# Optimization experiments

Measured on AMD Instinct MI355X. Metric: run time of the kernel, lower is better.

Reference implementation:

```python
import jax, jax.numpy as jnp
import numpy as np

N = 8192
NUM_FEAT = 512
NUM_HIDDENS = 128


def _mlp_params(key, fin, fh):
    k1, k2, k3, k4 = jax.random.split(key, 4)
    s1 = 1.0 / np.sqrt(fin)
    s2 = 1.0 / np.sqrt(fh)
    W1 = jax.random.uniform(k1, (fin, fh), jnp.float32, -s1, s1)
    b1 = jax.random.uniform(k2, (fh,), jnp.float32, -s1, s1)
    W2 = jax.random.uniform(k3, (fh, fh), jnp.float32, -s2, s2)
    b2 = jax.random.uniform(k4, (fh,), jnp.float32, -s2, s2)
    return W1, b1, W2, b2


def setup_inputs() -> dict:
    key = jax.random.key(0)
    ks = jax.random.split(key, 9)
    feat = jax.random.normal(ks[0], (N, NUM_FEAT), jnp.float32)
    adj = jax.random.uniform(ks[1], (N, N), jnp.float32)
    aa = jax.random.uniform(ks[2], (N, N), jnp.float32)
    mod = jax.random.normal(ks[3], (N, N), jnp.float32)
    Wl1, bl1, Wl2, bl2 = _mlp_params(ks[4], NUM_FEAT, NUM_HIDDENS)
    Wu1, bu1, Wu2, bu2 = _mlp_params(ks[5], NUM_FEAT, NUM_HIDDENS)
    Wa1, ba1, Wa2, ba2 = _mlp_params(ks[6], NUM_FEAT, NUM_HIDDENS)
    Wm1, bm1, Wm2, bm2 = _mlp_params(ks[7], NUM_FEAT, NUM_HIDDENS)
    ws = jnp.zeros((3,), jnp.float32)  # nn.init.zeros_(weighted_sum)
    return dict(feat=feat, adj=adj, aa=aa, mod=mod,
                Wl1=Wl1, bl1=bl1, Wl2=Wl2, bl2=bl2,
                Wu1=Wu1, bu1=bu1, Wu2=Wu2, bu2=bu2,
                Wa1=Wa1, ba1=ba1, Wa2=Wa2, ba2=ba2,
                Wm1=Wm1, bm1=bm1, Wm2=Wm2, bm2=bm2,
                ws=ws)


def _latent(feat, W1, b1, W2, b2):
    h = jax.nn.relu(feat @ W1 + b1)
    return h @ W2 + b2  # [N, H]


def reference(feat, adj, aa, mod,
              Wl1, bl1, Wl2, bl2,
              Wu1, bu1, Wu2, bu2,
              Wa1, ba1, Wa2, ba2,
              Wm1, bm1, Wm2, bm2, ws):
    lat_link = _latent(feat, Wl1, bl1, Wl2, bl2)
    lat_aa = _latent(feat, Wa1, ba1, Wa2, ba2)
    lat_mod = _latent(feat, Wm1, bm1, Wm2, bm2)
    lat_unlink = _latent(feat, Wu1, bu1, Wu2, bu2)

    link_ctx = jax.nn.sigmoid(lat_link @ lat_link.T)          # [N, N]
    aa_ctx = jax.nn.sigmoid((lat_aa @ lat_aa.T) * aa)         # [N, N]
    mod_ctx = jax.nn.sigmoid((lat_mod @ lat_mod.T) * mod)     # [N, N]

    w = jax.nn.softmax(ws)  # [3]
    # cat(..., dim=2) @ w  ==  weighted sum of the three contexts
    weight_link = w[0] * link_ctx + w[1] * aa_ctx + w[2] * mod_ctx

    weight_unlink = jax.nn.sigmoid(lat_unlink @ lat_unlink.T)
    return (weight_link - weight_unlink) * adj + weight_unlink
```

## Files before the change

### kernel.cpp

```cpp
#include <hip/hip_runtime.h>


typedef __attribute__((ext_vector_type(8))) short short8;
typedef __attribute__((ext_vector_type(4))) float f32x4;

__device__ __forceinline__ unsigned short f2bf(float x) {
  union { float f; unsigned u; } v; v.f = x;
  unsigned u = v.u + 0x7FFFu + ((v.u >> 16) & 1u);
  return (unsigned short)(u >> 16);
}

__device__ __forceinline__ float sigf(float x) {
  float e = __builtin_amdgcn_exp2f(-1.4426950408889634f * x);
  return __builtin_amdgcn_rcpf(1.0f + e);
}

__device__ __forceinline__ void gload_lds16u(const unsigned short* g, unsigned short* l) {
  __builtin_amdgcn_global_load_lds(
      (const __attribute__((address_space(1))) void*)g,
      (__attribute__((address_space(3))) void*)l, 16, 0, 0);
}

__device__ __forceinline__ unsigned lds_off(const void* p) {
  return (unsigned)(uintptr_t)(const __attribute__((address_space(3))) void*)p;
}
__device__ __forceinline__ short8 ds_read_frag(unsigned a) {
  short8 d;
  asm volatile("ds_read_b128 %0, %1" : "=v"(d) : "v"(a));
  return d;
}

__global__ __launch_bounds__(256) void k_featfrag(const float* __restrict__ feat,
                                                  unsigned short* __restrict__ dst) {
  int t = blockIdx.x * 256 + threadIdx.x;
  int row = t >> 6, kc = t & 63;
  const float4* s = reinterpret_cast<const float4*>(feat + row * 512 + kc * 8);
  float4 v0 = s[0], v1 = s[1];
  short8 o;
  o[0] = f2bf(v0.x); o[1] = f2bf(v0.y); o[2] = f2bf(v0.z); o[3] = f2bf(v0.w);
  o[4] = f2bf(v1.x); o[5] = f2bf(v1.y); o[6] = f2bf(v1.z); o[7] = f2bf(v1.w);
  int mb = row >> 4, kk = kc >> 2;
  int lane = ((kc & 3) << 4) | (row & 15);
  *reinterpret_cast<short8*>(dst + ((size_t)((mb * 16 + kk) * 64 + lane)) * 8) = o;
}

__global__ __launch_bounds__(256) void k_wfrag(
    const float* __restrict__ w1_0, const float* __restrict__ w1_1,
    const float* __restrict__ w1_2, const float* __restrict__ w1_3,
    const float* __restrict__ w2_0, const float* __restrict__ w2_1,
    const float* __restrict__ w2_2, const float* __restrict__ w2_3,
    unsigned short* __restrict__ w1f, unsigned short* __restrict__ w2f) {
  int t = blockIdx.x * 256 + threadIdx.x;
  if (t < 32768) {
    int lane = t & 63, nb = (t >> 6) & 7, kk = (t >> 9) & 15, g = t >> 13;
    const float* W = g == 0 ? w1_0 : g == 1 ? w1_1 : g == 2 ? w1_2 : w1_3;
    int q = lane >> 4, r = lane & 15;
    int col = nb * 16 + r;
    short8 o;
#pragma unroll
    for (int j = 0; j < 8; ++j) o[j] = f2bf(W[(kk * 32 + q * 8 + j) * 128 + col]);
    *reinterpret_cast<short8*>(w1f + (size_t)t * 8) = o;
  } else if (t < 40960) {
    int t2 = t - 32768;
    int lane = t2 & 63, nb = (t2 >> 6) & 7, kk = (t2 >> 9) & 3, g = t2 >> 11;
    const float* W = g == 0 ? w2_0 : g == 1 ? w2_1 : g == 2 ? w2_2 : w2_3;
    int q = lane >> 4, r = lane & 15;
    int col = nb * 16 + r;
    short8 o;
#pragma unroll
    for (int j = 0; j < 8; ++j) o[j] = f2bf(W[(kk * 32 + q * 8 + j) * 128 + col]);
    *reinterpret_cast<short8*>(w2f + (size_t)t2 * 8) = o;
  }
}

__global__ __launch_bounds__(256) void k_gemm1(
    const unsigned short* __restrict__ featf, const unsigned short* __restrict__ w1f,
    const float* __restrict__ b1_0, const float* __restrict__ b1_1,
    const float* __restrict__ b1_2, const float* __restrict__ b1_3,
    unsigned short* __restrict__ hfrag) {
  int bi = blockIdx.x, g = blockIdx.y;
  int lane = threadIdx.x & 63, w = threadIdx.x >> 6;
  int wm = w >> 1, wn = w & 1;
  int q = lane >> 4, r = lane & 15;
  int mbase = 8 * bi + 4 * wm;

  f32x4 s[4][4];
#pragma unroll
  for (int mi = 0; mi < 4; ++mi)
#pragma unroll
    for (int nj = 0; nj < 4; ++nj) s[mi][nj] = (f32x4){0.f, 0.f, 0.f, 0.f};

  for (int kk = 0; kk < 16; ++kk) {
    short8 a[4], b[4];
#pragma unroll
    for (int mi = 0; mi < 4; ++mi)
      a[mi] = *reinterpret_cast<const short8*>(
          featf + ((size_t)(((mbase + mi) * 16 + kk) * 64 + lane)) * 8);
#pragma unroll
    for (int nj = 0; nj < 4; ++nj)
      b[nj] = *reinterpret_cast<const short8*>(
          w1f + ((size_t)(((g * 16 + kk) * 8 + 4 * wn + nj) * 64 + lane)) * 8);
#pragma unroll
    for (int mi = 0; mi < 4; ++mi)
#pragma unroll
      for (int nj = 0; nj < 4; ++nj)
        s[mi][nj] = __builtin_amdgcn_mfma_f32_16x16x32_bf16(a[mi], b[nj], s[mi][nj], 0, 0, 0);
  }

  const float* b1 = g == 0 ? b1_0 : g == 1 ? b1_1 : g == 2 ? b1_2 : b1_3;
#pragma unroll
  for (int nj = 0; nj < 4; ++nj) {
    int cl = 64 * wn + 16 * nj + r;
    float bias = b1[cl];
    int Cg = 128 * g + cl;
    int kkd = Cg >> 5;
    int lane2hi = ((Cg >> 3) & 3) << 4;
    int j2 = Cg & 7;
#pragma unroll
    for (int mi = 0; mi < 4; ++mi) {
#pragma unroll
      for (int v = 0; v < 4; ++v) {
        int R = 128 * bi + 64 * wm + 16 * mi + 4 * q + v;
        float val = fmaxf(s[mi][nj][v] + bias, 0.0f);
        int mb = R >> 4;
        int lane2 = lane2hi | (R & 15);
        hfrag[((size_t)((mb * 16 + kkd) * 64 + lane2)) * 8 + j2] = f2bf(val);
      }
    }
  }
}

__global__ __launch_bounds__(256) void k_gemm2(
    const unsigned short* __restrict__ hfrag, const unsigned short* __restrict__ w2f,
    const float* __restrict__ b2_0, const float* __restrict__ b2_1,
    const float* __restrict__ b2_2, const float* __restrict__ b2_3,
    unsigned short* __restrict__ latf) {
  int bi = blockIdx.x, g = blockIdx.y;
  int lane = threadIdx.x & 63, w = threadIdx.x >> 6;
  int wm = w >> 1, wn = w & 1;
  int q = lane >> 4, r = lane & 15;
  int mbase = 8 * bi + 4 * wm;

  f32x4 s[4][4];
#pragma unroll
  for (int mi = 0; mi < 4; ++mi)
#pragma unroll
    for (int nj = 0; nj < 4; ++nj) s[mi][nj] = (f32x4){0.f, 0.f, 0.f, 0.f};

#pragma unroll
  for (int kk = 0; kk < 4; ++kk) {
    short8 a[4], b[4];
#pragma unroll
    for (int mi = 0; mi < 4; ++mi)
      a[mi] = *reinterpret_cast<const short8*>(
          hfrag + ((size_t)(((mbase + mi) * 16 + 4 * g + kk) * 64 + lane)) * 8);
#pragma unroll
    for (int nj = 0; nj < 4; ++nj)
      b[nj] = *reinterpret_cast<const short8*>(
          w2f + ((size_t)(((g * 4 + kk) * 8 + 4 * wn + nj) * 64 + lane)) * 8);
#pragma unroll
    for (int mi = 0; mi < 4; ++mi)
#pragma unroll
      for (int nj = 0; nj < 4; ++nj)
        s[mi][nj] = __builtin_amdgcn_mfma_f32_16x16x32_bf16(a[mi], b[nj], s[mi][nj], 0, 0, 0);
  }

  const float* b2 = g == 0 ? b2_0 : g == 1 ? b2_1 : g == 2 ? b2_2 : b2_3;
#pragma unroll
  for (int nj = 0; nj < 4; ++nj) {
    int cl = 64 * wn + 16 * nj + r;
    float bias = b2[cl];
    int kkd = cl >> 5;
    int lane2hi = ((cl >> 3) & 3) << 4;
    int j2 = cl & 7;
#pragma unroll
    for (int mi = 0; mi < 4; ++mi) {
#pragma unroll
      for (int v = 0; v < 4; ++v) {
        int R = 128 * bi + 64 * wm + 16 * mi + 4 * q + v;
        float val = s[mi][nj][v] + bias;
        int mb = R >> 4;
        int lane2 = lane2hi | (R & 15);
        latf[((size_t)(((g * 512 + mb) * 4 + kkd) * 64 + lane2)) * 8 + j2] = f2bf(val);
      }
    }
  }
}


#define VLD4(dst, p, OFF) \
  asm volatile("global_load_dwordx4 %0, %1, off offset:" OFF : "=v"(dst) : "v"(p))

#define LOADG(F, BASE, G)                                                     \
  do {                                                                        \
    const unsigned short* _p = (BASE) + (size_t)(G) * GS;                     \
    VLD4(F[0], _p, "0");    VLD4(F[1], _p, "1024");                           \
    VLD4(F[2], _p, "2048"); VLD4(F[3], _p, "3072");                           \
  } while (0)

#define GRAMG(SG, F, G)                                                       \
  do {                                                                        \
    short8 _i0 = ds_read_frag(fib + ((G) * 4 + 0) * 1024u + l16);             \
    short8 _i1 = ds_read_frag(fib + ((G) * 4 + 1) * 1024u + l16);             \
    short8 _i2 = ds_read_frag(fib + ((G) * 4 + 2) * 1024u + l16);             \
    short8 _i3 = ds_read_frag(fib + ((G) * 4 + 3) * 1024u + l16);             \
    asm volatile("s_waitcnt lgkmcnt(0)" ::: "memory");                        \
    __builtin_amdgcn_sched_barrier(0);                                        \
    SG = (f32x4){0.f, 0.f, 0.f, 0.f};                                         \
    SG = __builtin_amdgcn_mfma_f32_16x16x32_bf16(F[0], _i0, SG, 0, 0, 0);     \
    SG = __builtin_amdgcn_mfma_f32_16x16x32_bf16(F[1], _i1, SG, 0, 0, 0);     \
    SG = __builtin_amdgcn_mfma_f32_16x16x32_bf16(F[2], _i2, SG, 0, 0, 0);     \
    SG = __builtin_amdgcn_mfma_f32_16x16x32_bf16(F[3], _i3, SG, 0, 0, 0);     \
  } while (0)

#define STEP(S, EWCa, EWCm, EWCj, EWNa, EWNm, EWNj)                           \
  do {                                                                        \
    const unsigned short* fjbase =                                            \
        latf + (size_t)(cb0 + (S) * 4 + w) * 2048 + (size_t)lane * 8;         \
    f32x4 sg, o4;                                                             \
                                                     \
    LOADG(fjB, fjbase, 1);                                                    \
    asm volatile("s_waitcnt vmcnt(8)" ::: "memory");                          \
    __builtin_amdgcn_sched_barrier(0);                                        \
    GRAMG(sg, fjA, 0);                                                        \
    o4[0] = w0 * sigf(sg[0]); o4[1] = w0 * sigf(sg[1]);                       \
    o4[2] = w0 * sigf(sg[2]); o4[3] = w0 * sigf(sg[3]);                       \
                                                     \
    LOADG(fjA, fjbase, 2);                                                    \
    asm volatile("s_waitcnt vmcnt(4)" ::: "memory");                          \
    __builtin_amdgcn_sched_barrier(0);                                        \
    GRAMG(sg, fjB, 1);                                                        \
    o4[0] += w1 * sigf(sg[0] * EWCa[0]); o4[1] += w1 * sigf(sg[1] * EWCa[1]); \
    o4[2] += w1 * sigf(sg[2] * EWCa[2]); o4[3] += w1 * sigf(sg[3] * EWCa[3]); \
                                                     \
    LOADG(fjB, fjbase, 3);                                                    \
    asm volatile("s_waitcnt vmcnt(4)" ::: "memory");                          \
    __builtin_amdgcn_sched_barrier(0);                                        \
    GRAMG(sg, fjA, 2);                                                        \
    o4[0] += w2 * sigf(sg[0] * EWCm[0]); o4[1] += w2 * sigf(sg[1] * EWCm[1]); \
    o4[2] += w2 * sigf(sg[2] * EWCm[2]); o4[3] += w2 * sigf(sg[3] * EWCm[3]); \
                  \
    {                                                                         \
      const unsigned short* _nb = fjbase + 4 * 2048;    \
      LOADG(fjA, _nb, 0);                                                     \
      int _sn = ((S) + 1 < 32) ? (S) + 1 : (S);                               \
      const float* _ea = aa + ewoff + (size_t)_sn * 64;                       \
      const float* _em = mod + ewoff + (size_t)_sn * 64;                      \
      const float* _ej = adj + ewoff + (size_t)_sn * 64;                      \
      VLD4(EWNa, _ea, "0"); VLD4(EWNm, _em, "0"); VLD4(EWNj, _ej, "0");       \
    }                                                                         \
    asm volatile("s_waitcnt vmcnt(7)" ::: "memory");                          \
    __builtin_amdgcn_sched_barrier(0);                                        \
    GRAMG(sg, fjB, 3);                                                        \
    f32x4 res;                                                                \
    {                                                                         \
      float u0 = sigf(sg[0]), u1 = sigf(sg[1]);                               \
      float u2 = sigf(sg[2]), u3 = sigf(sg[3]);                               \
      res[0] = EWCj[0] * (o4[0] - u0) + u0;                                   \
      res[1] = EWCj[1] * (o4[1] - u1) + u1;                                   \
      res[2] = EWCj[2] * (o4[2] - u2) + u2;                                   \
      res[3] = EWCj[3] * (o4[3] - u3) + u3;                                   \
    }                                                                         \
    {                                                                         \
      float* _op = out + ewoff + (size_t)(S) * 64;                            \
      asm volatile("global_store_dwordx4 %0, %1, off" ::"v"(_op), "v"(res)    \
                   : "memory");                                               \
    }                                                                         \
  } while (0)

__global__ __launch_bounds__(256, 4) void k_ctx(
    const unsigned short* __restrict__ latf,
    const float* __restrict__ adj, const float* __restrict__ aa,
    const float* __restrict__ mod, const float* __restrict__ wsv,
    float* __restrict__ out) {
  __shared__ unsigned short fi_lds[8192];

  const int bid = blockIdx.x;
  const int cs = bid & 3;
  const int mb = bid >> 2;
  const int lane = threadIdx.x & 63, w = threadIdx.x >> 6;
  const int q = lane >> 4, r = lane & 15;

  float s0w = wsv[0], s1w = wsv[1], s2w = wsv[2];
  float mx = fmaxf(fmaxf(s0w, s1w), s2w);
  float e0 = __builtin_amdgcn_exp2f(1.4426950408889634f * (s0w - mx));
  float e1 = __builtin_amdgcn_exp2f(1.4426950408889634f * (s1w - mx));
  float e2 = __builtin_amdgcn_exp2f(1.4426950408889634f * (s2w - mx));
  float inv = __builtin_amdgcn_rcpf(e0 + e1 + e2);
  float w0 = e0 * inv, w1 = e1 * inv, w2 = e2 * inv;

  const size_t GS = (size_t)512 * 2048;
  const int cb0 = cs * 128;

  const size_t ewoff = (size_t)(mb * 16 + r) * 8192 + (size_t)cs * 2048
                     + (size_t)(16 * w + 4 * q);

#pragma unroll
  for (int kk = 0; kk < 4; ++kk)
    gload_lds16u(latf + GS * w + (size_t)(mb * 4 + kk) * 512 + lane * 8,
                 &fi_lds[(w * 4 + kk) * 512]);

  short8 fjA[4], fjB[4];
  f32x4 ewAa, ewAm, ewAj, ewBa, ewBm, ewBj;
  {
    const unsigned short* fjbase0 =
        latf + (size_t)(cb0 + w) * 2048 + (size_t)lane * 8;
    LOADG(fjA, fjbase0, 0);
  }
  VLD4(ewAa, (aa + ewoff), "0");
  VLD4(ewAm, (mod + ewoff), "0");
  VLD4(ewAj, (adj + ewoff), "0");
  asm volatile("s_waitcnt vmcnt(0)" ::: "memory");
  __builtin_amdgcn_s_barrier();

  const unsigned fib = lds_off(fi_lds);
  const unsigned l16 = (unsigned)lane * 16u;

#pragma unroll 1
  for (int s = 0; s < 32; s += 2) {
    STEP(s, ewAa, ewAm, ewAj, ewBa, ewBm, ewBj);
    STEP(s + 1, ewBa, ewBm, ewBj, ewAa, ewAm, ewAj);
  }
}

extern "C" void kernel_launch(void* const* d_in, const int* in_sizes, int n_in,
                              void* d_out, int out_size, void* d_ws, size_t ws_size,
                              hipStream_t stream) {
  const float* feat = (const float*)d_in[0];
  const float* adj  = (const float*)d_in[1];
  const float* aa   = (const float*)d_in[2];
  const float* mod  = (const float*)d_in[3];
  const float* W1g[4] = {(const float*)d_in[4], (const float*)d_in[12],
                         (const float*)d_in[16], (const float*)d_in[8]};
  const float* b1g[4] = {(const float*)d_in[5], (const float*)d_in[13],
                         (const float*)d_in[17], (const float*)d_in[9]};
  const float* W2g[4] = {(const float*)d_in[6], (const float*)d_in[14],
                         (const float*)d_in[18], (const float*)d_in[10]};
  const float* b2g[4] = {(const float*)d_in[7], (const float*)d_in[15],
                         (const float*)d_in[19], (const float*)d_in[11]};
  const float* wsv = (const float*)d_in[20];
  float* out = (float*)d_out;

  unsigned short* featf = (unsigned short*)d_ws;
  unsigned short* hfrag = featf + 4194304;
  unsigned short* latf  = hfrag + 4194304;
  unsigned short* w1f   = latf + 4194304;
  unsigned short* w2f   = w1f + 262144;
  if (ws_size < 25821184) return;

  k_featfrag<<<2048, 256, 0, stream>>>(feat, featf);
  k_wfrag<<<160, 256, 0, stream>>>(W1g[0], W1g[1], W1g[2], W1g[3],
                                   W2g[0], W2g[1], W2g[2], W2g[3], w1f, w2f);
  k_gemm1<<<dim3(64, 4), 256, 0, stream>>>(featf, w1f, b1g[0], b1g[1], b1g[2], b1g[3], hfrag);
  k_gemm2<<<dim3(64, 4), 256, 0, stream>>>(hfrag, w2f, b2g[0], b2g[1], b2g[2], b2g[3], latf);
  k_ctx<<<2048, 256, 0, stream>>>(latf, adj, aa, mod, wsv, out);
}
```

Measured before the change: 441.0 us.

## Keep row fragments in registers and stream shared column fragments through triple-buffered LDS

```diff
diff --git a/kernel.cpp b/kernel.cpp
--- a/kernel.cpp
+++ b/kernel.cpp
@@ -188,70 +188,57 @@
 }
 
 
+#define FILD(dst, p, OFF) \
+  asm volatile("global_load_dwordx4 %0, %1, off offset:" OFF : "=v"(dst) : "v"(p))
 #define VLD4(dst, p, OFF) \
   asm volatile("global_load_dwordx4 %0, %1, off offset:" OFF : "=v"(dst) : "v"(p))
 
-#define LOADG(F, BASE, G)                                                     \
+#define GRAMF(SG, G, FJC)                                                     \
   do {                                                                        \
-    const unsigned short* _p = (BASE) + (size_t)(G) * GS;                     \
-    VLD4(F[0], _p, "0");    VLD4(F[1], _p, "1024");                           \
-    VLD4(F[2], _p, "2048"); VLD4(F[3], _p, "3072");                           \
-  } while (0)
-
-#define GRAMG(SG, F, G)                                                       \
-  do {                                                                        \
-    short8 _i0 = ds_read_frag(fib + ((G) * 4 + 0) * 1024u + l16);             \
-    short8 _i1 = ds_read_frag(fib + ((G) * 4 + 1) * 1024u + l16);             \
-    short8 _i2 = ds_read_frag(fib + ((G) * 4 + 2) * 1024u + l16);             \
-    short8 _i3 = ds_read_frag(fib + ((G) * 4 + 3) * 1024u + l16);             \
+    short8 _j0 = ds_read_frag((FJC) + ((G) * 4 + 0) * 1024u + l16);           \
+    short8 _j1 = ds_read_frag((FJC) + ((G) * 4 + 1) * 1024u + l16);           \
+    short8 _j2 = ds_read_frag((FJC) + ((G) * 4 + 2) * 1024u + l16);           \
+    short8 _j3 = ds_read_frag((FJC) + ((G) * 4 + 3) * 1024u + l16);           \
     asm volatile("s_waitcnt lgkmcnt(0)" ::: "memory");                        \
     __builtin_amdgcn_sched_barrier(0);                                        \
     SG = (f32x4){0.f, 0.f, 0.f, 0.f};                                         \
-    SG = __builtin_amdgcn_mfma_f32_16x16x32_bf16(F[0], _i0, SG, 0, 0, 0);     \
-    SG = __builtin_amdgcn_mfma_f32_16x16x32_bf16(F[1], _i1, SG, 0, 0, 0);     \
-    SG = __builtin_amdgcn_mfma_f32_16x16x32_bf16(F[2], _i2, SG, 0, 0, 0);     \
-    SG = __builtin_amdgcn_mfma_f32_16x16x32_bf16(F[3], _i3, SG, 0, 0, 0);     \
+    SG = __builtin_amdgcn_mfma_f32_16x16x32_bf16(_j0, fi[G][0], SG, 0, 0, 0); \
+    SG = __builtin_amdgcn_mfma_f32_16x16x32_bf16(_j1, fi[G][1], SG, 0, 0, 0); \
+    SG = __builtin_amdgcn_mfma_f32_16x16x32_bf16(_j2, fi[G][2], SG, 0, 0, 0); \
+    SG = __builtin_amdgcn_mfma_f32_16x16x32_bf16(_j3, fi[G][3], SG, 0, 0, 0); \
   } while (0)
 
 #define STEP(S, EWCa, EWCm, EWCj, EWNa, EWNm, EWNj)                           \
   do {                                                                        \
-    const unsigned short* fjbase =                                            \
-        latf + (size_t)(cb0 + (S) * 4 + w) * 2048 + (size_t)lane * 8;         \
+    int _bf = (br == 2) ? 0 : br + 1;                                         \
+    int _sn = ((S) < 63) ? (S) + 1 : 63;                                      \
+    {                                                                         \
+      const unsigned short* _fp = latf + GS * w                               \
+          + ((size_t)((tj0 + _sn) * 4) << 9) + (size_t)lane * 8;              \
+      gload_lds16u(_fp,        &fj_lds[_bf][w * 4 + 0][0]);                   \
+      gload_lds16u(_fp + 512,  &fj_lds[_bf][w * 4 + 1][0]);                   \
+      gload_lds16u(_fp + 1024, &fj_lds[_bf][w * 4 + 2][0]);                   \
+      gload_lds16u(_fp + 1536, &fj_lds[_bf][w * 4 + 3][0]);                   \
+      VLD4(EWNa, (aa + ewoff + (size_t)_sn * 16), "0");                       \
+      VLD4(EWNm, (mod + ewoff + (size_t)_sn * 16), "0");                      \
+      VLD4(EWNj, (adj + ewoff + (size_t)_sn * 16), "0");                      \
+    }                                                                         \
+    __builtin_amdgcn_sched_barrier(0);                                        \
+          \
+    asm volatile("s_waitcnt vmcnt(7)" ::: "memory");                          \
+    __builtin_amdgcn_s_barrier();                                             \
+    const unsigned _fjc = fjb + (unsigned)br * 16384u;                        \
     f32x4 sg, o4;                                                             \
-                                                     \
-    LOADG(fjB, fjbase, 1);                                                    \
-    asm volatile("s_waitcnt vmcnt(8)" ::: "memory");                          \
-    __builtin_amdgcn_sched_barrier(0);                                        \
-    GRAMG(sg, fjA, 0);                                                        \
+    GRAMF(sg, 0, _fjc);                                                       \
     o4[0] = w0 * sigf(sg[0]); o4[1] = w0 * sigf(sg[1]);                       \
     o4[2] = w0 * sigf(sg[2]); o4[3] = w0 * sigf(sg[3]);                       \
-                                                     \
-    LOADG(fjA, fjbase, 2);                                                    \
-    asm volatile("s_waitcnt vmcnt(4)" ::: "memory");                          \
-    __builtin_amdgcn_sched_barrier(0);                                        \
-    GRAMG(sg, fjB, 1);                                                        \
+    GRAMF(sg, 1, _fjc);                                                       \
     o4[0] += w1 * sigf(sg[0] * EWCa[0]); o4[1] += w1 * sigf(sg[1] * EWCa[1]); \
     o4[2] += w1 * sigf(sg[2] * EWCa[2]); o4[3] += w1 * sigf(sg[3] * EWCa[3]); \
-                                                     \
-    LOADG(fjB, fjbase, 3);                                                    \
-    asm volatile("s_waitcnt vmcnt(4)" ::: "memory");                          \
-    __builtin_amdgcn_sched_barrier(0);                                        \
-    GRAMG(sg, fjA, 2);                                                        \
+    GRAMF(sg, 2, _fjc);                                                       \
     o4[0] += w2 * sigf(sg[0] * EWCm[0]); o4[1] += w2 * sigf(sg[1] * EWCm[1]); \
     o4[2] += w2 * sigf(sg[2] * EWCm[2]); o4[3] += w2 * sigf(sg[3] * EWCm[3]); \
-                  \
-    {                                                                         \
-      const unsigned short* _nb = fjbase + 4 * 2048;    \
-      LOADG(fjA, _nb, 0);                                                     \
-      int _sn = ((S) + 1 < 32) ? (S) + 1 : (S);                               \
-      const float* _ea = aa + ewoff + (size_t)_sn * 64;                       \
-      const float* _em = mod + ewoff + (size_t)_sn * 64;                      \
-      const float* _ej = adj + ewoff + (size_t)_sn * 64;                      \
-      VLD4(EWNa, _ea, "0"); VLD4(EWNm, _em, "0"); VLD4(EWNj, _ej, "0");       \
-    }                                                                         \
-    asm volatile("s_waitcnt vmcnt(7)" ::: "memory");                          \
-    __builtin_amdgcn_sched_barrier(0);                                        \
-    GRAMG(sg, fjB, 3);                                                        \
+    GRAMF(sg, 3, _fjc);                                                       \
     f32x4 res;                                                                \
     {                                                                         \
       float u0 = sigf(sg[0]), u1 = sigf(sg[1]);                               \
@@ -262,24 +249,26 @@
       res[3] = EWCj[3] * (o4[3] - u3) + u3;                                   \
     }                                                                         \
     {                                                                         \
-      float* _op = out + ewoff + (size_t)(S) * 64;                            \
+      float* _op = out + ewoff + (size_t)(S) * 16;                            \
       asm volatile("global_store_dwordx4 %0, %1, off" ::"v"(_op), "v"(res)    \
                    : "memory");                                               \
     }                                                                         \
+    br = _bf;                                                                 \
   } while (0)
 
-__global__ __launch_bounds__(256, 4) void k_ctx(
+__global__ __launch_bounds__(256, 3) void k_ctx(
     const unsigned short* __restrict__ latf,
     const float* __restrict__ adj, const float* __restrict__ aa,
     const float* __restrict__ mod, const float* __restrict__ wsv,
     float* __restrict__ out) {
-  __shared__ unsigned short fi_lds[8192];
+  __shared__ unsigned short fj_lds[3][16][512];
 
   const int bid = blockIdx.x;
-  const int cs = bid & 3;
-  const int mb = bid >> 2;
+  const int cs = bid & 7;
+  const int rb = bid >> 3;
   const int lane = threadIdx.x & 63, w = threadIdx.x >> 6;
   const int q = lane >> 4, r = lane & 15;
+  const int mb = rb * 4 + w;
 
   float s0w = wsv[0], s1w = wsv[1], s2w = wsv[2];
   float mx = fmaxf(fmaxf(s0w, s1w), s2w);
@@ -290,34 +279,48 @@
   float w0 = e0 * inv, w1 = e1 * inv, w2 = e2 * inv;
 
   const size_t GS = (size_t)512 * 2048;
-  const int cb0 = cs * 128;
-
-  const size_t ewoff = (size_t)(mb * 16 + r) * 8192 + (size_t)cs * 2048
-                     + (size_t)(16 * w + 4 * q);
-
-#pragma unroll
-  for (int kk = 0; kk < 4; ++kk)
-    gload_lds16u(latf + GS * w + (size_t)(mb * 4 + kk) * 512 + lane * 8,
-                 &fi_lds[(w * 4 + kk) * 512]);
-
-  short8 fjA[4], fjB[4];
+  const int tj0 = cs * 64;
+
+  const size_t ewoff = (size_t)(mb * 16 + r) * 8192 + (size_t)cs * 1024
+                     + (size_t)(4 * q);
+
+  short8 fi[4][4];
+  {
+    const unsigned short* p0 = latf + ((size_t)(mb * 4) << 9) + (size_t)lane * 8;
+    FILD(fi[0][0], p0, "0");    FILD(fi[0][1], p0, "1024");
+    FILD(fi[0][2], p0, "2048"); FILD(fi[0][3], p0, "3072");
+    p0 += GS;
+    FILD(fi[1][0], p0, "0");    FILD(fi[1][1], p0, "1024");
+    FILD(fi[1][2], p0, "2048"); FILD(fi[1][3], p0, "3072");
+    p0 += GS;
+    FILD(fi[2][0], p0, "0");    FILD(fi[2][1], p0, "1024");
+    FILD(fi[2][2], p0, "2048"); FILD(fi[2][3], p0, "3072");
+    p0 += GS;
+    FILD(fi[3][0], p0, "0");    FILD(fi[3][1], p0, "1024");
+    FILD(fi[3][2], p0, "2048"); FILD(fi[3][3], p0, "3072");
+  }
+
+  {
+    const unsigned short* fp = latf + GS * w
+        + ((size_t)(tj0 * 4) << 9) + (size_t)lane * 8;
+    gload_lds16u(fp,        &fj_lds[0][w * 4 + 0][0]);
+    gload_lds16u(fp + 512,  &fj_lds[0][w * 4 + 1][0]);
+    gload_lds16u(fp + 1024, &fj_lds[0][w * 4 + 2][0]);
+    gload_lds16u(fp + 1536, &fj_lds[0][w * 4 + 3][0]);
+  }
   f32x4 ewAa, ewAm, ewAj, ewBa, ewBm, ewBj;
-  {
-    const unsigned short* fjbase0 =
-        latf + (size_t)(cb0 + w) * 2048 + (size_t)lane * 8;
-    LOADG(fjA, fjbase0, 0);
-  }
   VLD4(ewAa, (aa + ewoff), "0");
   VLD4(ewAm, (mod + ewoff), "0");
   VLD4(ewAj, (adj + ewoff), "0");
   asm volatile("s_waitcnt vmcnt(0)" ::: "memory");
   __builtin_amdgcn_s_barrier();
 
-  const unsigned fib = lds_off(fi_lds);
+  const unsigned fjb = lds_off(fj_lds);
   const unsigned l16 = (unsigned)lane * 16u;
+  int br = 0;
 
 #pragma unroll 1
-  for (int s = 0; s < 32; s += 2) {
+  for (int s = 0; s < 64; s += 2) {
     STEP(s, ewAa, ewAm, ewAj, ewBa, ewBm, ewBj);
     STEP(s + 1, ewBa, ewBm, ewBj, ewAa, ewAm, ewAj);
   }
@@ -353,5 +356,5 @@
                                    W2g[0], W2g[1], W2g[2], W2g[3], w1f, w2f);
   k_gemm1<<<dim3(64, 4), 256, 0, stream>>>(featf, w1f, b1g[0], b1g[1], b1g[2], b1g[3], hfrag);
   k_gemm2<<<dim3(64, 4), 256, 0, stream>>>(hfrag, w2f, b2g[0], b2g[1], b2g[2], b2g[3], latf);
-  k_ctx<<<2048, 256, 0, stream>>>(latf, adj, aa, mod, wsv, out);
-}
+  k_ctx<<<1024, 256, 0, stream>>>(latf, adj, aa, mod, wsv, out);
+}
```

Measured after the change: 370.4 us. 1.19x faster.
